# Kernel tuning notes

Hardware: AMD Instinct MI355X
Metric: run time of the kernel (lower is better)

The kernel has to match this reference:

```python
import jax, jax.numpy as jnp
import numpy as np

DATA_WIDTH = 8  # fixed-point data width; bitstream length L = 2**DATA_WIDTH


def gen_bitstream(x, rng, data_width):
    """Vectorized GenBitstreamGroup.

    For each element x: if x == 0 -> Zero flag set, all-zero bitstream.
    Otherwise normalize |x| into [0.5, 1) via leftShift (number of left
    shifts), then unary-encode the normalized value against the RNG
    sequence: bit_t = 1 iff rng[t] < floor(norm * L).
    Returns (bits [..., L], leftShift [...], zero [...]).
    """
    L = rng.shape[0]
    zero = (x == 0)
    ax = jnp.abs(x)
    safe = jnp.where(zero, jnp.float32(1.0), ax)
    # leftShift: smallest s >= 0 with |x| * 2**s in [0.5, 1)
    s = jnp.clip(jnp.floor(-jnp.log2(safe)), 0.0, jnp.float32(data_width))
    norm = ax * jnp.exp2(s)                       # normalized magnitude in [0.5, 1]
    thresh = jnp.floor(norm * L)                  # integer threshold in [0, L]
    bits = (rng.astype(jnp.float32)[None, None, :] < thresh[:, :, None]).astype(jnp.float32)
    bits = jnp.where(zero[:, :, None], jnp.float32(0.0), bits)
    return bits, s, zero


def setup_inputs() -> dict:
    key = jax.random.key(0)
    k1, k2 = jax.random.split(key)
    M, K, N = 256, 256, 256
    L = 2 ** DATA_WIDTH
    tensor_1 = jax.random.uniform(k1, (M, K), dtype=jnp.float32)
    tensor_2 = jax.random.uniform(k2, (K, N), dtype=jnp.float32)
    rngSeq = jnp.arange(L, dtype=jnp.int32)
    return {"tensor_1": tensor_1, "tensor_2": tensor_2, "rngSeq": rngSeq}


def reference(tensor_1, tensor_2, rngSeq):
    L = rngSeq.shape[0]
    ascending = jnp.arange(L, dtype=jnp.int32)  # module's ascendingSeq for tensor_2
    b1, s1, z1 = gen_bitstream(tensor_1, rngSeq, DATA_WIDTH)      # [M,K,L]
    b2, s2, z2 = gen_bitstream(tensor_2, ascending, DATA_WIDTH)   # [K,N,L]
    # BitstreamMUL: AND the two bitstreams, popcount, rescale by bitstream
    # length and undo the normalization left-shifts.
    count = jnp.einsum('mkl,knl->mnk', b1, b2)                    # [M,N,K] popcounts
    scale = jnp.exp2(-(s1[:, None, :] + s2.T[None, :, :])) / L    # [M,N,K]
    valid = ((~z1)[:, None, :] & (~z2).T[None, :, :]).astype(jnp.float32)
    sgn = jnp.sign(tensor_1)[:, None, :] * jnp.sign(tensor_2).T[None, :, :]
    sc = count * scale * valid * sgn                              # per-k SC products
    return sc.sum(axis=-1)                                        # [M,N] result
```

## Files before the change

### kernel.cpp

```cpp
#include <hip/hip_runtime.h>


constexpr int DIM = 256;
constexpr int MK  = DIM * DIM;

__global__ __launch_bounds__(256) void precomp_kernel(
    const float* __restrict__ x1, const float* __restrict__ x2,
    float* __restrict__ T1, float* __restrict__ A1,
    float* __restrict__ T2, float* __restrict__ A2)
{
    int i = blockIdx.x * 256 + threadIdx.x;
    const float* src;
    float *T, *A;
    int j;
    if (i < MK) { src = x1; T = T1; A = A1; j = i; }
    else        { src = x2; T = T2; A = A2; j = i - MK; }

    float v  = src[j];
    float ax = fabsf(v);
    float t, a;
    if (ax == 0.0f) {
        t = 0.0f; a = 0.0f;
    } else {
        float s = floorf(-log2f(ax));
        s = fminf(fmaxf(s, 0.0f), 8.0f);
        t = floorf(ax * exp2f(s) * 256.0f);
        a = copysignf(exp2f(-s), v);
    }
    T[j] = t;
    A[j] = a;
}

__global__ __launch_bounds__(256) void scgemm_kernel(
    const float* __restrict__ T1, const float* __restrict__ A1,
    const float* __restrict__ T2, const float* __restrict__ A2,
    float* __restrict__ out)
{
    __shared__ float sT[DIM];
    __shared__ float sA[DIM];
    const int m = blockIdx.x;
    const int n = threadIdx.x;

    sT[n] = T1[m * DIM + n];
    sA[n] = A1[m * DIM + n];
    __syncthreads();

    float acc = 0.0f;
    #pragma unroll 8
    for (int k = 0; k < DIM; ++k) {
        float t2 = T2[k * DIM + n];
        float a2 = A2[k * DIM + n];
        acc = fmaf(fminf(sT[k], t2), sA[k] * a2, acc);
    }
    out[m * DIM + n] = acc * (1.0f / 256.0f);
}

extern "C" void kernel_launch(void* const* d_in, const int* in_sizes, int n_in,
                              void* d_out, int out_size, void* d_ws, size_t ws_size,
                              hipStream_t stream)
{
    const float* x1 = (const float*)d_in[0];
    const float* x2 = (const float*)d_in[1];

    float* ws = (float*)d_ws;
    float* T1 = ws;
    float* A1 = ws + MK;
    float* T2 = ws + 2 * MK;
    float* A2 = ws + 3 * MK;
    float* out = (float*)d_out;

    hipLaunchKernelGGL(precomp_kernel, dim3(2 * MK / 256), dim3(256), 0, stream,
                       x1, x2, T1, A1, T2, A2);
    hipLaunchKernelGGL(scgemm_kernel, dim3(DIM), dim3(256), 0, stream,
                       T1, A1, T2, A2, out);
}
```

Measured before the change: 69.75 us.

## Pack threshold and scale into one word, fuse x1 prep, split K across waves

Each element's threshold and power-of-two scale are now packed into one 32-bit word, computed with bit manipulation instead of log2/exp2. This halves the workspace traffic for the second operand. The first operand's packing moves into the GEMM kernel, so precompute only handles tensor_2. The GEMM block grows to 1024 threads, splits K into four chunks and reduces the partial sums through shared memory, which raises parallelism per block but adds a second barrier.

```diff
diff --git a/kernel.cpp b/kernel.cpp
--- a/kernel.cpp
+++ b/kernel.cpp
@@ -4,55 +4,65 @@
 constexpr int DIM = 256;
 constexpr int MK  = DIM * DIM;
 
-__global__ __launch_bounds__(256) void precomp_kernel(
-    const float* __restrict__ x1, const float* __restrict__ x2,
-    float* __restrict__ T1, float* __restrict__ A1,
-    float* __restrict__ T2, float* __restrict__ A2)
+__device__ inline unsigned pack_sc(float v) {
+    unsigned ub = __float_as_uint(v);
+    unsigned ax = ub & 0x7fffffffu;
+    if (ax == 0u) return 0u;
+    int B        = (int)(ax >> 23);
+    unsigned mnt = ax & 0x7fffffu;
+    int s = 126 - B + (mnt == 0u ? 1 : 0);
+    s = s < 0 ? 0 : (s > 8 ? 8 : s);
+    float scaled = __uint_as_float(ax) * __uint_as_float((unsigned)(127 + s + 8) << 23);
+    unsigned t = (unsigned)scaled;
+    t = t > 256u ? 256u : t;
+    unsigned fb = (ub & 0x80000000u) | ((unsigned)(127 - s) << 23);
+    return (fb & 0xFFFF0000u) | t;
+}
+
+__global__ __launch_bounds__(256) void precomp2_kernel(
+    const float* __restrict__ x2, unsigned* __restrict__ P2)
 {
     int i = blockIdx.x * 256 + threadIdx.x;
-    const float* src;
-    float *T, *A;
-    int j;
-    if (i < MK) { src = x1; T = T1; A = A1; j = i; }
-    else        { src = x2; T = T2; A = A2; j = i - MK; }
-
-    float v  = src[j];
-    float ax = fabsf(v);
-    float t, a;
-    if (ax == 0.0f) {
-        t = 0.0f; a = 0.0f;
-    } else {
-        float s = floorf(-log2f(ax));
-        s = fminf(fmaxf(s, 0.0f), 8.0f);
-        t = floorf(ax * exp2f(s) * 256.0f);
-        a = copysignf(exp2f(-s), v);
-    }
-    T[j] = t;
-    A[j] = a;
+    P2[i] = pack_sc(x2[i]);
 }
 
-__global__ __launch_bounds__(256) void scgemm_kernel(
-    const float* __restrict__ T1, const float* __restrict__ A1,
-    const float* __restrict__ T2, const float* __restrict__ A2,
+__global__ __launch_bounds__(1024) void scgemm_kernel(
+    const float* __restrict__ x1, const unsigned* __restrict__ P2,
     float* __restrict__ out)
 {
-    __shared__ float sT[DIM];
-    __shared__ float sA[DIM];
-    const int m = blockIdx.x;
-    const int n = threadIdx.x;
+    __shared__ unsigned sT[DIM];
+    __shared__ float    sF[DIM];
+    __shared__ float    part[4][DIM];
 
-    sT[n] = T1[m * DIM + n];
-    sA[n] = A1[m * DIM + n];
+    const int tid = threadIdx.x;
+    const int m   = blockIdx.x;
+    const int n   = tid & (DIM - 1);
+    const int kc  = tid >> 8;
+
+    if (tid < DIM) {
+        unsigned p = pack_sc(x1[m * DIM + tid]);
+        sT[tid] = p & 0xFFFFu;
+        sF[tid] = __uint_as_float(p & 0xFFFF0000u);
+    }
     __syncthreads();
 
     float acc = 0.0f;
+    const int kbase = kc * 64;
     #pragma unroll 8
-    for (int k = 0; k < DIM; ++k) {
-        float t2 = T2[k * DIM + n];
-        float a2 = A2[k * DIM + n];
-        acc = fmaf(fminf(sT[k], t2), sA[k] * a2, acc);
+    for (int kk = 0; kk < 64; ++kk) {
+        const int k  = kbase + kk;
+        unsigned u2  = P2[k * DIM + n];
+        unsigned t2  = u2 & 0xFFFFu;
+        float    f2  = __uint_as_float(u2 & 0xFFFF0000u);
+        unsigned c   = min(sT[k], t2);
+        acc = fmaf((float)c, sF[k] * f2, acc);
     }
-    out[m * DIM + n] = acc * (1.0f / 256.0f);
+    part[kc][n] = acc;
+    __syncthreads();
+    if (tid < DIM) {
+        float r = part[0][tid] + part[1][tid] + part[2][tid] + part[3][tid];
+        out[m * DIM + tid] = r * (1.0f / 256.0f);
+    }
 }
 
 extern "C" void kernel_launch(void* const* d_in, const int* in_sizes, int n_in,
@@ -62,15 +72,9 @@
     const float* x1 = (const float*)d_in[0];
     const float* x2 = (const float*)d_in[1];
 
-    float* ws = (float*)d_ws;
-    float* T1 = ws;
-    float* A1 = ws + MK;
-    float* T2 = ws + 2 * MK;
-    float* A2 = ws + 3 * MK;
-    float* out = (float*)d_out;
+    unsigned* P2  = (unsigned*)d_ws;
+    float*    out = (float*)d_out;
 
-    hipLaunchKernelGGL(precomp_kernel, dim3(2 * MK / 256), dim3(256), 0, stream,
-                       x1, x2, T1, A1, T2, A2);
-    hipLaunchKernelGGL(scgemm_kernel, dim3(DIM), dim3(256), 0, stream,
-                       T1, A1, T2, A2, out);
+    hipLaunchKernelGGL(precomp2_kernel, dim3(MK / 256), dim3(256), 0, stream, x2, P2);
+    hipLaunchKernelGGL(scgemm_kernel, dim3(DIM), dim3(1024), 0, stream, x1, P2, out);
 }
```

Result: faster. 62.46 us (-10.4%).
